# Optimization experiments

Measured on AMD Instinct MI355X. Metric: run time of the kernel, lower is better.

The kernel has to match this reference:

```python
import jax, jax.numpy as jnp
import numpy as np

B, S, D, H = 2, 2048, 1024, 16
DK = D // H


def setup_inputs() -> dict:
    key = jax.random.key(0)
    ks = jax.random.split(key, 8)
    w_scale = 1.0 / np.sqrt(D)
    return {
        "query": jax.random.normal(ks[0], (B, S, D), jnp.float32),
        "key": jax.random.normal(ks[1], (B, S, D), jnp.float32),
        "value": jax.random.normal(ks[2], (B, S, D), jnp.float32),
        "Wq": jax.random.normal(ks[3], (D, D), jnp.float32) * w_scale,
        "bq": jnp.zeros((D,), jnp.float32),
        "Wk": jax.random.normal(ks[4], (D, D), jnp.float32) * w_scale,
        "bk": jnp.zeros((D,), jnp.float32),
        "Wv": jax.random.normal(ks[5], (D, D), jnp.float32) * w_scale,
        "bv": jnp.zeros((D,), jnp.float32),
        "Wo": jax.random.normal(ks[6], (D, D), jnp.float32) * w_scale,
        "bo": jnp.zeros((D,), jnp.float32),
    }


def _heads(x, W, b):
    # torch nn.Linear: y = x @ W.T + b ; then [B,S,D] -> [B,H,S,DK]
    y = x @ W.T + b
    return y.reshape(x.shape[0], x.shape[1], H, DK).transpose(0, 2, 1, 3)


def reference(query, key, value, Wq, bq, Wk, bk, Wv, bv, Wo, bo):
    q = _heads(query, Wq, bq)   # [B,H,S,DK]
    k = _heads(key, Wk, bk)
    v = _heads(value, Wv, bv)
    scale = 100.0 / np.sqrt(DK).astype(np.float32)
    scores = jnp.einsum("bhqd,bhkd->bhqk", q, k) * scale  # [B,H,Sq,Sk]
    prob = jax.nn.softmax(scores, axis=-1)                 # dropout p=0 -> identity
    out = jnp.einsum("bhqk,bhkd->bhqd", prob, v)           # [B,H,Sq,DK]
    mean_atp = prob.mean(axis=(1, 2))                      # mean over heads & query -> [B,Sk]
    out = out.transpose(0, 2, 1, 3).reshape(query.shape[0], -1, D)
    out = out @ Wo.T + bo
    return out, mean_atp
```

## Files before the change

kernel.cpp:

```cpp
#include <hip/hip_runtime.h>
#include <hip/hip_bf16.h>


#define B_  2
#define S_  2048
#define D_  1024
#define H_  16
#define DK_ 64

typedef __bf16 bf16x8 __attribute__((ext_vector_type(8)));
typedef float f32x4  __attribute__((ext_vector_type(4)));

__device__ __forceinline__ void ld_g2l16(const __bf16* g, __bf16* l) {
  __builtin_amdgcn_global_load_lds(
      (const __attribute__((address_space(1))) void*)g,
      (__attribute__((address_space(3))) void*)l, 16, 0, 0);
}

__device__ __forceinline__ void split3_body(const float* __restrict__ x,
                                            __bf16* __restrict__ y,
                                            int lbid, int tid, int mode)
{
  int i = (lbid * 256 + tid) * 8;
  float4 a = *(const float4*)(x + i);
  float4 b = *(const float4*)(x + i + 4);
  float xs[8] = {a.x, a.y, a.z, a.w, b.x, b.y, b.z, b.w};
  __bf16 out[24];
#pragma unroll
  for (int j = 0; j < 8; j++) {
    float v = xs[j];
    __bf16 hi = (__bf16)v;
    __bf16 lo = (__bf16)(v - (float)hi);
    if (mode == 0) { out[3*j] = hi; out[3*j+1] = hi; out[3*j+2] = lo; }
    else           { out[3*j] = hi; out[3*j+1] = lo; out[3*j+2] = hi; }
  }
  *(bf16x8*)(y + 3 * (size_t)i)      = *(bf16x8*)&out[0];
  *(bf16x8*)(y + 3 * (size_t)i + 8)  = *(bf16x8*)&out[8];
  *(bf16x8*)(y + 3 * (size_t)i + 16) = *(bf16x8*)&out[16];
}

__device__ __forceinline__ void tobf16_body(const float* __restrict__ x,
                                            __bf16* __restrict__ y,
                                            int lbid, int tid)
{
  int i = (lbid * 256 + tid) * 8;
  float4 a = *(const float4*)(x + i);
  float4 b = *(const float4*)(x + i + 4);
  __bf16 out[8] = {(__bf16)a.x, (__bf16)a.y, (__bf16)a.z, (__bf16)a.w,
                   (__bf16)b.x, (__bf16)b.y, (__bf16)b.z, (__bf16)b.w};
  *(bf16x8*)(y + i) = *(bf16x8*)&out[0];
}

__global__ __launch_bounds__(256)
void convert_all(const float* __restrict__ query, const float* __restrict__ key_,
                 const float* __restrict__ value, const float* __restrict__ Wq,
                 const float* __restrict__ Wk, const float* __restrict__ Wv,
                 const float* __restrict__ Wo, __bf16* __restrict__ qcat3,
                 __bf16* __restrict__ kcat3, __bf16* __restrict__ vxb,
                 __bf16* __restrict__ wqc3, __bf16* __restrict__ wkc3,
                 __bf16* __restrict__ wvb, __bf16* __restrict__ wob,
                 float* __restrict__ atp)
{
  int bid = blockIdx.x, tid = threadIdx.x;
  if (bid < 2048)       split3_body(query, qcat3, bid, tid, 0);
  else if (bid < 4096)  split3_body(key_,  kcat3, bid - 2048, tid, 0);
  else if (bid < 6144)  tobf16_body(value, vxb,   bid - 4096, tid);
  else if (bid < 6656)  split3_body(Wq, wqc3, bid - 6144, tid, 1);
  else if (bid < 7168)  split3_body(Wk, wkc3, bid - 6656, tid, 1);
  else if (bid < 7680)  tobf16_body(Wv, wvb, bid - 7168, tid);
  else if (bid < 8192)  tobf16_body(Wo, wob, bid - 7680, tid);
  else {
    int base = (bid - 8192) * 2048;
#pragma unroll
    for (int j = 0; j < 8; j++) atp[base + j * 256 + tid] = 0.f;
  }
}

#define TM 64
#define TN 128
#define TK 64

__device__ __forceinline__
void gemm_body(const __bf16* __restrict__ X, const __bf16* __restrict__ W,
               const float* __restrict__ bias, void* __restrict__ Y,
               void* __restrict__ Y2, int N, int K, int out_mode, float osf,
               __bf16* Xa, __bf16* Wb, int bx, int by)
{
  const int tid  = threadIdx.x;
  const int lane = tid & 63;
  const int w    = tid >> 6;
  const int c    = lane & 15;
  const int quad = lane >> 4;
  const int row0 = by * TM;
  const int col0 = bx * TN;
  const int wc   = w * 32;

  f32x4 acc[4][2];
#pragma unroll
  for (int i = 0; i < 4; i++)
#pragma unroll
    for (int j = 0; j < 2; j++) acc[i][j] = (f32x4){0.f, 0.f, 0.f, 0.f};

  for (int k0 = 0; k0 < K; k0 += TK) {
    __syncthreads();
#pragma unroll
    for (int i = 0; i < 2; i++) {
      int chunk = i * 256 + w * 64 + lane;
      int r = chunk >> 3, dch = chunk & 7;
      ld_g2l16(X + (size_t)(row0 + r) * K + k0 + dch * 8, &Xa[chunk * 8]);
    }
#pragma unroll
    for (int i = 0; i < 4; i++) {
      int chunk = i * 256 + w * 64 + lane;
      int r = chunk >> 3, dch = chunk & 7;
      ld_g2l16(W + (size_t)(col0 + r) * K + k0 + dch * 8, &Wb[chunk * 8]);
    }
    __syncthreads();

#pragma unroll
    for (int cc = 0; cc < 2; cc++) {
      bf16x8 af[4], bf[2];
#pragma unroll
      for (int i = 0; i < 4; i++)
        af[i] = *(const bf16x8*)&Xa[(i * 16 + c) * TK + cc * 32 + quad * 8];
#pragma unroll
      for (int j = 0; j < 2; j++)
        bf[j] = *(const bf16x8*)&Wb[(wc + j * 16 + c) * TK + cc * 32 + quad * 8];
#pragma unroll
      for (int i = 0; i < 4; i++)
#pragma unroll
        for (int j = 0; j < 2; j++)
          acc[i][j] = __builtin_amdgcn_mfma_f32_16x16x32_bf16(af[i], bf[j],
                                                              acc[i][j], 0, 0, 0);
    }
  }

#pragma unroll
  for (int i = 0; i < 4; i++) {
#pragma unroll
    for (int j = 0; j < 2; j++) {
      int col = col0 + wc + j * 16 + c;
      float bcol = bias[col];
#pragma unroll
      for (int r = 0; r < 4; r++) {
        int row = row0 + i * 16 + quad * 4 + r;
        float v = (acc[i][j][r] + bcol) * osf;
        if (out_mode == 0) {
          ((float*)Y)[(size_t)row * N + col] = v;
        } else {
          int b2 = row >> 11, s = row & (S_ - 1);
          int h = col >> 6, dk = col & 63;
          if (out_mode == 1) {
            size_t off = ((size_t)(b2 * H_ + h) * S_ + s) * DK_ + dk;
            __bf16 hi = (__bf16)v;
            ((__bf16*)Y)[off]  = hi;
            ((__bf16*)Y2)[off] = (__bf16)(v - (float)hi);
          } else {
            ((__bf16*)Y)[((size_t)(b2 * H_ + h) * DK_ + dk) * S_ + s] = (__bf16)v;
          }
        }
      }
    }
  }
}

__global__ __launch_bounds__(256)
void gemm_qkv(const __bf16* __restrict__ qcat3, const __bf16* __restrict__ wqc3,
              const float* __restrict__ bq, __bf16* __restrict__ qh, __bf16* __restrict__ ql,
              const __bf16* __restrict__ kcat3, const __bf16* __restrict__ wkc3,
              const float* __restrict__ bk, __bf16* __restrict__ kh, __bf16* __restrict__ kl,
              const __bf16* __restrict__ vxb, const __bf16* __restrict__ wvb,
              const float* __restrict__ bv, __bf16* __restrict__ vt, float qsf)
{
  __shared__ __align__(16) __bf16 Xa[TM * TK];
  __shared__ __align__(16) __bf16 Wb[TN * TK];
  int z = blockIdx.z;
  if (z == 0)
    gemm_body(qcat3, wqc3, bq, qh, ql, D_, 3 * D_, 1, qsf, Xa, Wb, blockIdx.x, blockIdx.y);
  else if (z == 1)
    gemm_body(kcat3, wkc3, bk, kh, kl, D_, 3 * D_, 1, 1.0f, Xa, Wb, blockIdx.x, blockIdx.y);
  else
    gemm_body(vxb, wvb, bv, vt, nullptr, D_, D_, 2, 1.0f, Xa, Wb, blockIdx.x, blockIdx.y);
}

__global__ __launch_bounds__(256)
void gemm_mfma(const __bf16* __restrict__ X, const __bf16* __restrict__ W,
               const float* __restrict__ bias, void* __restrict__ Y,
               void* __restrict__ Y2, int M, int N, int K, int out_mode,
               float osf)
{
  __shared__ __align__(16) __bf16 Xa[TM * TK];
  __shared__ __align__(16) __bf16 Wb[TN * TK];
  gemm_body(X, W, bias, Y, Y2, N, K, out_mode, osf, Xa, Wb, blockIdx.x, blockIdx.y);
}

#define LSTR 72
#define PSTR 68

__device__ __forceinline__ void qk_scores(const __bf16* __restrict__ Kh,
                                          const __bf16* __restrict__ Kl,
                                          const bf16x8 qhf[2],
                                          const bf16x8 qlf[2],
                                          int c, int quad, f32x4 sc[4])
{
#pragma unroll
  for (int nt = 0; nt < 4; nt++) {
    sc[nt] = (f32x4){0.f, 0.f, 0.f, 0.f};
#pragma unroll
    for (int cc = 0; cc < 2; cc++) {
      bf16x8 bh8 = *(const bf16x8*)&Kh[(nt * 16 + c) * LSTR + cc * 32 + quad * 8];
      bf16x8 bl8 = *(const bf16x8*)&Kl[(nt * 16 + c) * LSTR + cc * 32 + quad * 8];
      sc[nt] = __builtin_amdgcn_mfma_f32_16x16x32_bf16(qhf[cc], bh8, sc[nt], 0, 0, 0);
      sc[nt] = __builtin_amdgcn_mfma_f32_16x16x32_bf16(qhf[cc], bl8, sc[nt], 0, 0, 0);
      sc[nt] = __builtin_amdgcn_mfma_f32_16x16x32_bf16(qlf[cc], bh8, sc[nt], 0, 0, 0);
    }
  }
}

__global__ __launch_bounds__(512)
void attn_mfma(const __bf16* __restrict__ qh_ws, const __bf16* __restrict__ ql_ws,
               const __bf16* __restrict__ kh_ws, const __bf16* __restrict__ kl_ws,
               const __bf16* __restrict__ vt_ws, __bf16* __restrict__ attn_out,
               float* __restrict__ atp_out)
{
  __shared__ __align__(16) __bf16 Kh[64 * LSTR];
  __shared__ __align__(16) __bf16 Kl[64 * LSTR];
  __shared__ __align__(16) __bf16 Vt[64 * LSTR];
  __shared__ __align__(16) float  Ps[8][16 * PSTR];
  __shared__ float  atp_lds[S_];

  const int tid  = threadIdx.x;
  const int lane = tid & 63;
  const int w    = tid >> 6;
  const int c    = lane & 15;
  const int quad = lane >> 4;
  const int qb   = blockIdx.x;
  const int h    = blockIdx.y;
  const int b    = blockIdx.z;

  const size_t bh = (size_t)(b * H_ + h);
  const __bf16* qhg = qh_ws + (bh * S_ + qb * 128) * DK_;
  const __bf16* qlg = ql_ws + (bh * S_ + qb * 128) * DK_;
  const __bf16* khg = kh_ws + bh * S_ * DK_;
  const __bf16* klg = kl_ws + bh * S_ * DK_;
  const __bf16* vg  = vt_ws + bh * DK_ * S_;

  bf16x8 qhf[2], qlf[2];
  {
    const __bf16* qrow = qhg + (size_t)(w * 16 + c) * DK_;
    qhf[0] = *(const bf16x8*)(qrow + quad * 8);
    qhf[1] = *(const bf16x8*)(qrow + 32 + quad * 8);
    const __bf16* qrow2 = qlg + (size_t)(w * 16 + c) * DK_;
    qlf[0] = *(const bf16x8*)(qrow2 + quad * 8);
    qlf[1] = *(const bf16x8*)(qrow2 + 32 + quad * 8);
  }

  float m_r[4], l_r[4];
#pragma unroll
  for (int r = 0; r < 4; r++) { m_r[r] = -1e30f; l_r[r] = 0.f; }

  for (int kt = 0; kt < S_ / 64; kt++) {
    __syncthreads();
    {
      int key = tid >> 3, dch = tid & 7;
      *(bf16x8*)&Kh[key * LSTR + dch * 8] =
          *(const bf16x8*)(khg + (size_t)(kt * 64 + key) * DK_ + dch * 8);
      *(bf16x8*)&Kl[key * LSTR + dch * 8] =
          *(const bf16x8*)(klg + (size_t)(kt * 64 + key) * DK_ + dch * 8);
    }
    __syncthreads();

    f32x4 sc[4];
    qk_scores(Kh, Kl, qhf, qlf, c, quad, sc);

    float tm[4], psum[4];
#pragma unroll
    for (int r = 0; r < 4; r++)
      tm[r] = fmaxf(fmaxf(sc[0][r], sc[1][r]), fmaxf(sc[2][r], sc[3][r]));
#pragma unroll
    for (int o = 1; o < 16; o <<= 1)
#pragma unroll
      for (int r = 0; r < 4; r++)
        tm[r] = fmaxf(tm[r], __shfl_xor(tm[r], o, 64));

#pragma unroll
    for (int r = 0; r < 4; r++) {
      float mnew = fmaxf(m_r[r], tm[r]);
      float p = 0.f;
#pragma unroll
      for (int nt = 0; nt < 4; nt++) p += exp2f(sc[nt][r] - mnew);
      psum[r] = p;
      l_r[r] *= exp2f(m_r[r] - mnew);
      m_r[r] = mnew;
    }
#pragma unroll
    for (int o = 1; o < 16; o <<= 1)
#pragma unroll
      for (int r = 0; r < 4; r++)
        psum[r] += __shfl_xor(psum[r], o, 64);
#pragma unroll
    for (int r = 0; r < 4; r++) l_r[r] += psum[r];
  }

  float z_r[4];
#pragma unroll
  for (int r = 0; r < 4; r++) z_r[r] = m_r[r] + log2f(l_r[r]);

  for (int i = tid; i < S_; i += 512) atp_lds[i] = 0.f;

  f32x4 of[4];
#pragma unroll
  for (int nt = 0; nt < 4; nt++) of[nt] = (f32x4){0.f, 0.f, 0.f, 0.f};

  float* ps = Ps[w];

  for (int kt = 0; kt < S_ / 64; kt++) {
    __syncthreads();
    {
      int key = tid >> 3, dch = tid & 7;
      *(bf16x8*)&Kh[key * LSTR + dch * 8] =
          *(const bf16x8*)(khg + (size_t)(kt * 64 + key) * DK_ + dch * 8);
      *(bf16x8*)&Kl[key * LSTR + dch * 8] =
          *(const bf16x8*)(klg + (size_t)(kt * 64 + key) * DK_ + dch * 8);
      *(bf16x8*)&Vt[key * LSTR + dch * 8] =
          *(const bf16x8*)(vg + (size_t)key * S_ + kt * 64 + dch * 8);
    }
    __syncthreads();

    f32x4 sc[4];
    qk_scores(Kh, Kl, qhf, qlf, c, quad, sc);

    float t[4];
#pragma unroll
    for (int nt = 0; nt < 4; nt++) {
      t[nt] = 0.f;
#pragma unroll
      for (int r = 0; r < 4; r++) {
        float p = exp2f(sc[nt][r] - z_r[r]);
        ps[(quad * 4 + r) * PSTR + nt * 16 + c] = p;
        t[nt] += p;
      }
    }

    bf16x8 pa[2];
#pragma unroll
    for (int cc = 0; cc < 2; cc++) {
      const float* pp = &ps[c * PSTR + cc * 32 + quad * 8];
      f32x4 p0 = *(const f32x4*)pp;
      f32x4 p1 = *(const f32x4*)(pp + 4);
      bf16x8 v8;
#pragma unroll
      for (int j = 0; j < 4; j++) { v8[j] = (__bf16)p0[j]; v8[4 + j] = (__bf16)p1[j]; }
      pa[cc] = v8;
    }
#pragma unroll
    for (int nt = 0; nt < 4; nt++)
#pragma unroll
      for (int cc = 0; cc < 2; cc++) {
        bf16x8 vb = *(const bf16x8*)&Vt[(nt * 16 + c) * LSTR + cc * 32 + quad * 8];
        of[nt] = __builtin_amdgcn_mfma_f32_16x16x32_bf16(pa[cc], vb, of[nt], 0, 0, 0);
      }

#pragma unroll
    for (int nt = 0; nt < 4; nt++) {
      float tt = t[nt];
      tt += __shfl_xor(tt, 16, 64);
      tt += __shfl_xor(tt, 32, 64);
      if (quad == 0) atomicAdd(&atp_lds[kt * 64 + nt * 16 + c], tt);
    }
  }

#pragma unroll
  for (int nt = 0; nt < 4; nt++)
#pragma unroll
    for (int r = 0; r < 4; r++)
      attn_out[((size_t)(b * S_ + qb * 128 + w * 16 + quad * 4 + r)) * D_
               + h * DK_ + nt * 16 + c] = (__bf16)of[nt][r];

  __syncthreads();
  const float inv = 1.0f / ((float)H_ * (float)S_);
  for (int i = tid; i < S_; i += 512)
    atomicAdd(&atp_out[b * S_ + i], atp_lds[i] * inv);
}

extern "C" void kernel_launch(void* const* d_in, const int* in_sizes, int n_in,
                              void* d_out, int out_size, void* d_ws, size_t ws_size,
                              hipStream_t stream)
{
  const float* query = (const float*)d_in[0];
  const float* key_  = (const float*)d_in[1];
  const float* value = (const float*)d_in[2];
  const float* Wq = (const float*)d_in[3];
  const float* bq = (const float*)d_in[4];
  const float* Wk = (const float*)d_in[5];
  const float* bk = (const float*)d_in[6];
  const float* Wv = (const float*)d_in[7];
  const float* bv = (const float*)d_in[8];
  const float* Wo = (const float*)d_in[9];
  const float* bo = (const float*)d_in[10];

  float* out = (float*)d_out;
  float* atp = out + (size_t)B_ * S_ * D_;

  const size_t NE = (size_t)B_ * S_ * D_;
  const size_t NW = (size_t)D_ * D_;
  __bf16* p = (__bf16*)d_ws;
  __bf16* qcat3 = p;               p += 3 * NE;
  __bf16* kcat3 = p;               p += 3 * NE;
  __bf16* wqc3  = p;               p += 3 * NW;
  __bf16* wkc3  = p;               p += 3 * NW;
  __bf16* vxb   = p;               p += NE;
  __bf16* wvb   = p;               p += NW;
  __bf16* wob   = p;               p += NW;
  __bf16* qh_ws = p;               p += NE;
  __bf16* ql_ws = p;               p += NE;
  __bf16* kh_ws = p;               p += NE;
  __bf16* kl_ws = p;               p += NE;
  __bf16* vt_ws = kcat3;
  __bf16* a_ws  = qcat3;

  const int M = B_ * S_;
  const float QSF = 18.0337320f;

  convert_all<<<8194, 256, 0, stream>>>(query, key_, value, Wq, Wk, Wv, Wo,
                                        qcat3, kcat3, vxb, wqc3, wkc3, wvb, wob,
                                        atp);

  gemm_qkv<<<dim3(D_ / TN, M / TM, 3), 256, 0, stream>>>(
      qcat3, wqc3, bq, qh_ws, ql_ws,
      kcat3, wkc3, bk, kh_ws, kl_ws,
      vxb,   wvb,  bv, vt_ws, QSF);

  attn_mfma<<<dim3(S_ / 128, H_, B_), 512, 0, stream>>>(qh_ws, ql_ws, kh_ws, kl_ws,
                                                        vt_ws, a_ws, atp);

  gemm_mfma<<<dim3(D_ / TN, M / TM), 256, 0, stream>>>(a_ws, wob, bo, out, nullptr,
                                                       M, D_, D_, 0, 1.0f);
}
```

Measured before the change: 480.7 us.

## Fuse PV into online-softmax pass; cheap bf16-only second pass for attention means

Restructures attention so the first pass is a full online-softmax flash loop that accumulates P·V with rescaling. A second pass then recomputes scores using only the high bf16 part of Q and K to accumulate the mean attention probabilities. P is now staged in LDS as packed bf16 instead of fp32, and a min-blocks hint is added to launch bounds. This cuts the second pass's MFMA and LDS traffic, at the risk of lower accuracy in the mean probabilities, since the scores are scaled by 100 and the lo-part correction is dropped.

```diff
diff --git a/kernel.cpp b/kernel.cpp
--- a/kernel.cpp
+++ b/kernel.cpp
@@ -9,6 +9,7 @@
 #define DK_ 64
 
 typedef __bf16 bf16x8 __attribute__((ext_vector_type(8)));
+typedef __bf16 bf16x2 __attribute__((ext_vector_type(2)));
 typedef float f32x4  __attribute__((ext_vector_type(4)));
 
 __device__ __forceinline__ void ld_g2l16(const __bf16* g, __bf16* l) {
@@ -194,30 +195,10 @@
   gemm_body(X, W, bias, Y, Y2, N, K, out_mode, osf, Xa, Wb, blockIdx.x, blockIdx.y);
 }
 
-#define LSTR 72
-#define PSTR 68
-
-__device__ __forceinline__ void qk_scores(const __bf16* __restrict__ Kh,
-                                          const __bf16* __restrict__ Kl,
-                                          const bf16x8 qhf[2],
-                                          const bf16x8 qlf[2],
-                                          int c, int quad, f32x4 sc[4])
-{
-#pragma unroll
-  for (int nt = 0; nt < 4; nt++) {
-    sc[nt] = (f32x4){0.f, 0.f, 0.f, 0.f};
-#pragma unroll
-    for (int cc = 0; cc < 2; cc++) {
-      bf16x8 bh8 = *(const bf16x8*)&Kh[(nt * 16 + c) * LSTR + cc * 32 + quad * 8];
-      bf16x8 bl8 = *(const bf16x8*)&Kl[(nt * 16 + c) * LSTR + cc * 32 + quad * 8];
-      sc[nt] = __builtin_amdgcn_mfma_f32_16x16x32_bf16(qhf[cc], bh8, sc[nt], 0, 0, 0);
-      sc[nt] = __builtin_amdgcn_mfma_f32_16x16x32_bf16(qhf[cc], bl8, sc[nt], 0, 0, 0);
-      sc[nt] = __builtin_amdgcn_mfma_f32_16x16x32_bf16(qlf[cc], bh8, sc[nt], 0, 0, 0);
-    }
-  }
-}
-
-__global__ __launch_bounds__(512)
+#define LSTR  72
+#define PBSTR 72
+
+__global__ __launch_bounds__(512, 6)
 void attn_mfma(const __bf16* __restrict__ qh_ws, const __bf16* __restrict__ ql_ws,
                const __bf16* __restrict__ kh_ws, const __bf16* __restrict__ kl_ws,
                const __bf16* __restrict__ vt_ws, __bf16* __restrict__ attn_out,
@@ -226,7 +207,7 @@
   __shared__ __align__(16) __bf16 Kh[64 * LSTR];
   __shared__ __align__(16) __bf16 Kl[64 * LSTR];
   __shared__ __align__(16) __bf16 Vt[64 * LSTR];
-  __shared__ __align__(16) float  Ps[8][16 * PSTR];
+  __shared__ __align__(16) __bf16 Ps[8][16 * PBSTR];
   __shared__ float  atp_lds[S_];
 
   const int tid  = threadIdx.x;
@@ -259,123 +240,145 @@
 #pragma unroll
   for (int r = 0; r < 4; r++) { m_r[r] = -1e30f; l_r[r] = 0.f; }
 
+  f32x4 of[4];
+#pragma unroll
+  for (int nt = 0; nt < 4; nt++) of[nt] = (f32x4){0.f, 0.f, 0.f, 0.f};
+
+  __bf16* ps = Ps[w];
+  const bool evenc = (c & 1) == 0;
+  const int kb2 = c & ~1;
+  const int rw0 = evenc ? 0 : 2;
+
+  for (int kt = 0; kt < S_ / 64; kt++) {
+    __syncthreads();
+    {
+      int key = tid >> 3, dch = tid & 7;
+      size_t goff = (size_t)(kt * 64 + key) * DK_ + dch * 8;
+      *(bf16x8*)&Kh[key * LSTR + dch * 8] = *(const bf16x8*)(khg + goff);
+      *(bf16x8*)&Kl[key * LSTR + dch * 8] = *(const bf16x8*)(klg + goff);
+      *(bf16x8*)&Vt[key * LSTR + dch * 8] =
+          *(const bf16x8*)(vg + (size_t)key * S_ + kt * 64 + dch * 8);
+    }
+    __syncthreads();
+
+    f32x4 sc[4];
+#pragma unroll
+    for (int nt = 0; nt < 4; nt++) {
+      sc[nt] = (f32x4){0.f, 0.f, 0.f, 0.f};
+#pragma unroll
+      for (int cc = 0; cc < 2; cc++) {
+        bf16x8 bh8 = *(const bf16x8*)&Kh[(nt * 16 + c) * LSTR + cc * 32 + quad * 8];
+        bf16x8 bl8 = *(const bf16x8*)&Kl[(nt * 16 + c) * LSTR + cc * 32 + quad * 8];
+        sc[nt] = __builtin_amdgcn_mfma_f32_16x16x32_bf16(qhf[cc], bh8, sc[nt], 0, 0, 0);
+        sc[nt] = __builtin_amdgcn_mfma_f32_16x16x32_bf16(qhf[cc], bl8, sc[nt], 0, 0, 0);
+        sc[nt] = __builtin_amdgcn_mfma_f32_16x16x32_bf16(qlf[cc], bh8, sc[nt], 0, 0, 0);
+      }
+    }
+
+    float tm[4];
+#pragma unroll
+    for (int r = 0; r < 4; r++)
+      tm[r] = fmaxf(fmaxf(sc[0][r], sc[1][r]), fmaxf(sc[2][r], sc[3][r]));
+#pragma unroll
+    for (int o = 1; o < 16; o <<= 1)
+#pragma unroll
+      for (int r = 0; r < 4; r++)
+        tm[r] = fmaxf(tm[r], __shfl_xor(tm[r], o, 64));
+
+    float alpha[4];
+#pragma unroll
+    for (int r = 0; r < 4; r++) {
+      float mnew = fmaxf(m_r[r], tm[r]);
+      alpha[r] = exp2f(m_r[r] - mnew);
+      m_r[r] = mnew;
+    }
+
+    float psum[4] = {0.f, 0.f, 0.f, 0.f};
+#pragma unroll
+    for (int nt = 0; nt < 4; nt++) {
+      float p[4], pq[4];
+#pragma unroll
+      for (int r = 0; r < 4; r++) {
+        p[r] = exp2f(sc[nt][r] - m_r[r]);
+        psum[r] += p[r];
+      }
+#pragma unroll
+      for (int r = 0; r < 4; r++) pq[r] = __shfl_xor(p[r], 1, 64);
+#pragma unroll
+      for (int rr = 0; rr < 2; rr++) {
+        int r = rw0 + rr;
+        bf16x2 pk;
+        pk[0] = evenc ? (__bf16)p[r]  : (__bf16)pq[r];
+        pk[1] = evenc ? (__bf16)pq[r] : (__bf16)p[r];
+        *(bf16x2*)&ps[(quad * 4 + r) * PBSTR + nt * 16 + kb2] = pk;
+      }
+    }
+#pragma unroll
+    for (int o = 1; o < 16; o <<= 1)
+#pragma unroll
+      for (int r = 0; r < 4; r++)
+        psum[r] += __shfl_xor(psum[r], o, 64);
+#pragma unroll
+    for (int r = 0; r < 4; r++) l_r[r] = l_r[r] * alpha[r] + psum[r];
+
+#pragma unroll
+    for (int nt = 0; nt < 4; nt++)
+#pragma unroll
+      for (int r = 0; r < 4; r++) of[nt][r] *= alpha[r];
+
+    bf16x8 pa[2];
+#pragma unroll
+    for (int cc = 0; cc < 2; cc++)
+      pa[cc] = *(const bf16x8*)&ps[c * PBSTR + cc * 32 + quad * 8];
+#pragma unroll
+    for (int nt = 0; nt < 4; nt++)
+#pragma unroll
+      for (int cc = 0; cc < 2; cc++) {
+        bf16x8 vb = *(const bf16x8*)&Vt[(nt * 16 + c) * LSTR + cc * 32 + quad * 8];
+        of[nt] = __builtin_amdgcn_mfma_f32_16x16x32_bf16(pa[cc], vb, of[nt], 0, 0, 0);
+      }
+  }
+
+  float z_r[4];
+#pragma unroll
+  for (int r = 0; r < 4; r++) {
+    z_r[r] = m_r[r] + log2f(l_r[r]);
+    l_r[r] = 1.0f / l_r[r];
+  }
+#pragma unroll
+  for (int nt = 0; nt < 4; nt++)
+#pragma unroll
+    for (int r = 0; r < 4; r++)
+      attn_out[((size_t)(b * S_ + qb * 128 + w * 16 + quad * 4 + r)) * D_
+               + h * DK_ + nt * 16 + c] = (__bf16)(of[nt][r] * l_r[r]);
+
+  for (int i = tid; i < S_; i += 512) atp_lds[i] = 0.f;
+
   for (int kt = 0; kt < S_ / 64; kt++) {
     __syncthreads();
     {
       int key = tid >> 3, dch = tid & 7;
       *(bf16x8*)&Kh[key * LSTR + dch * 8] =
           *(const bf16x8*)(khg + (size_t)(kt * 64 + key) * DK_ + dch * 8);
-      *(bf16x8*)&Kl[key * LSTR + dch * 8] =
-          *(const bf16x8*)(klg + (size_t)(kt * 64 + key) * DK_ + dch * 8);
-    }
-    __syncthreads();
-
-    f32x4 sc[4];
-    qk_scores(Kh, Kl, qhf, qlf, c, quad, sc);
-
-    float tm[4], psum[4];
-#pragma unroll
-    for (int r = 0; r < 4; r++)
-      tm[r] = fmaxf(fmaxf(sc[0][r], sc[1][r]), fmaxf(sc[2][r], sc[3][r]));
-#pragma unroll
-    for (int o = 1; o < 16; o <<= 1)
-#pragma unroll
-      for (int r = 0; r < 4; r++)
-        tm[r] = fmaxf(tm[r], __shfl_xor(tm[r], o, 64));
-
-#pragma unroll
-    for (int r = 0; r < 4; r++) {
-      float mnew = fmaxf(m_r[r], tm[r]);
-      float p = 0.f;
-#pragma unroll
-      for (int nt = 0; nt < 4; nt++) p += exp2f(sc[nt][r] - mnew);
-      psum[r] = p;
-      l_r[r] *= exp2f(m_r[r] - mnew);
-      m_r[r] = mnew;
-    }
-#pragma unroll
-    for (int o = 1; o < 16; o <<= 1)
-#pragma unroll
-      for (int r = 0; r < 4; r++)
-        psum[r] += __shfl_xor(psum[r], o, 64);
-#pragma unroll
-    for (int r = 0; r < 4; r++) l_r[r] += psum[r];
-  }
-
-  float z_r[4];
-#pragma unroll
-  for (int r = 0; r < 4; r++) z_r[r] = m_r[r] + log2f(l_r[r]);
-
-  for (int i = tid; i < S_; i += 512) atp_lds[i] = 0.f;
-
-  f32x4 of[4];
-#pragma unroll
-  for (int nt = 0; nt < 4; nt++) of[nt] = (f32x4){0.f, 0.f, 0.f, 0.f};
-
-  float* ps = Ps[w];
-
-  for (int kt = 0; kt < S_ / 64; kt++) {
-    __syncthreads();
-    {
-      int key = tid >> 3, dch = tid & 7;
-      *(bf16x8*)&Kh[key * LSTR + dch * 8] =
-          *(const bf16x8*)(khg + (size_t)(kt * 64 + key) * DK_ + dch * 8);
-      *(bf16x8*)&Kl[key * LSTR + dch * 8] =
-          *(const bf16x8*)(klg + (size_t)(kt * 64 + key) * DK_ + dch * 8);
-      *(bf16x8*)&Vt[key * LSTR + dch * 8] =
-          *(const bf16x8*)(vg + (size_t)key * S_ + kt * 64 + dch * 8);
-    }
-    __syncthreads();
-
-    f32x4 sc[4];
-    qk_scores(Kh, Kl, qhf, qlf, c, quad, sc);
-
-    float t[4];
+    }
+    __syncthreads();
+
 #pragma unroll
     for (int nt = 0; nt < 4; nt++) {
-      t[nt] = 0.f;
-#pragma unroll
-      for (int r = 0; r < 4; r++) {
-        float p = exp2f(sc[nt][r] - z_r[r]);
-        ps[(quad * 4 + r) * PSTR + nt * 16 + c] = p;
-        t[nt] += p;
-      }
-    }
-
-    bf16x8 pa[2];
-#pragma unroll
-    for (int cc = 0; cc < 2; cc++) {
-      const float* pp = &ps[c * PSTR + cc * 32 + quad * 8];
-      f32x4 p0 = *(const f32x4*)pp;
-      f32x4 p1 = *(const f32x4*)(pp + 4);
-      bf16x8 v8;
-#pragma unroll
-      for (int j = 0; j < 4; j++) { v8[j] = (__bf16)p0[j]; v8[4 + j] = (__bf16)p1[j]; }
-      pa[cc] = v8;
-    }
-#pragma unroll
-    for (int nt = 0; nt < 4; nt++)
+      f32x4 sc = {0.f, 0.f, 0.f, 0.f};
 #pragma unroll
       for (int cc = 0; cc < 2; cc++) {
-        bf16x8 vb = *(const bf16x8*)&Vt[(nt * 16 + c) * LSTR + cc * 32 + quad * 8];
-        of[nt] = __builtin_amdgcn_mfma_f32_16x16x32_bf16(pa[cc], vb, of[nt], 0, 0, 0);
-      }
-
-#pragma unroll
-    for (int nt = 0; nt < 4; nt++) {
-      float tt = t[nt];
-      tt += __shfl_xor(tt, 16, 64);
-      tt += __shfl_xor(tt, 32, 64);
-      if (quad == 0) atomicAdd(&atp_lds[kt * 64 + nt * 16 + c], tt);
-    }
-  }
-
-#pragma unroll
-  for (int nt = 0; nt < 4; nt++)
-#pragma unroll
-    for (int r = 0; r < 4; r++)
-      attn_out[((size_t)(b * S_ + qb * 128 + w * 16 + quad * 4 + r)) * D_
-               + h * DK_ + nt * 16 + c] = (__bf16)of[nt][r];
+        bf16x8 bh8 = *(const bf16x8*)&Kh[(nt * 16 + c) * LSTR + cc * 32 + quad * 8];
+        sc = __builtin_amdgcn_mfma_f32_16x16x32_bf16(qhf[cc], bh8, sc, 0, 0, 0);
+      }
+      float t = 0.f;
+#pragma unroll
+      for (int r = 0; r < 4; r++) t += exp2f(sc[r] - z_r[r]);
+      t += __shfl_xor(t, 16, 64);
+      t += __shfl_xor(t, 32, 64);
+      if (quad == 0) atomicAdd(&atp_lds[kt * 64 + nt * 16 + c], t);
+    }
+  }
 
   __syncthreads();
   const float inv = 1.0f / ((float)H_ * (float)S_);
```

Result: slower. 659.4 us (+37.2%).
